# Kernel tuning notes

Hardware: AMD Instinct MI355X
Metric: run time of the kernel (lower is better)

## Reference

```python
import jax, jax.numpy as jnp
import numpy as np

N_NODES = 100000
N_EDGES = 1600000
HIDDEN = 128
HALF = HIDDEN // 2
LN_EPS = 1e-5


def setup_inputs() -> dict:
    key = jax.random.key(0)
    ks = jax.random.split(key, 8)
    pos = jax.random.normal(ks[0], (N_NODES, 3), dtype=jnp.float32) * 10.0
    edge_index = jax.random.randint(ks[1], (2, N_EDGES), 0, N_NODES, dtype=jnp.int64)
    batch = jnp.zeros((N_NODES,), dtype=jnp.int64)
    # spatial_encoder params: Linear(3, HALF) -> LayerNorm(HALF) -> GELU -> Linear(HALF, HALF)
    W1 = jax.random.normal(ks[2], (3, HALF), dtype=jnp.float32) * 0.3
    b1 = jax.random.normal(ks[3], (HALF,), dtype=jnp.float32) * 0.05
    ln_g = jnp.ones((HALF,), dtype=jnp.float32)
    ln_b = jnp.zeros((HALF,), dtype=jnp.float32)
    W2 = jax.random.normal(ks[4], (HALF, HALF), dtype=jnp.float32) * 0.1
    b2 = jax.random.normal(ks[5], (HALF,), dtype=jnp.float32) * 0.05
    return {"pos": pos, "edge_index": edge_index, "batch": batch,
            "W1": W1, "b1": b1, "ln_g": ln_g, "ln_b": ln_b, "W2": W2, "b2": b2}


def _layernorm(x, g, b):
    mu = jnp.mean(x, axis=-1, keepdims=True)
    var = jnp.mean((x - mu) ** 2, axis=-1, keepdims=True)
    return (x - mu) * jax.lax.rsqrt(var + LN_EPS) * g + b


def reference(pos, edge_index, batch, W1, b1, ln_g, ln_b, W2, b2):
    num_nodes = pos.shape[0]
    src, dst = edge_index[0], edge_index[1]
    rel = pos[dst] - pos[src]                              # [E, 3]
    dist = jnp.linalg.norm(rel, axis=1, keepdims=True)     # [E, 1]
    rel_n = rel / (dist + 1e-6)
    h = rel_n @ W1 + b1                                    # [E, HALF]
    h = _layernorm(h, ln_g, ln_b)
    h = jax.nn.gelu(h, approximate=False)                  # torch exact GELU
    code = h @ W2 + b2                                     # dropout is identity in eval
    agg = jax.ops.segment_sum(code, dst, num_segments=num_nodes)          # [N, HALF]
    deg = jax.ops.segment_sum(jnp.ones_like(dst, dtype=code.dtype), dst,
                              num_segments=num_nodes)
    deg = jnp.clip(deg, 1.0)
    agg = agg / deg[:, None]
    # original buffer is [N, HIDDEN]; only the first HALF channels receive updates
    out = jnp.concatenate([agg, jnp.zeros_like(agg)], axis=1)             # [N, HIDDEN]
    return out
```

## Files before the change

kernel.cpp:

```cpp
#include <hip/hip_runtime.h>
#include <math.h>

#define HALF 64
#define LN_EPS 1e-5f
#define SA_CAP 640

#define GC0 -2.3022082f
#define GC1 -0.1029438f

__device__ __forceinline__ float gelu_fast(float x) {
    const float x2 = x * x;
    const float z  = x * fmaf(GC1, x2, GC0);
    const float e  = __builtin_amdgcn_exp2f(z);
    const float sg = __builtin_amdgcn_rcpf(1.0f + e);
    return x * sg;
}

__global__ void __launch_bounds__(256) hist_kernel(
    const int* __restrict__ dst, int* __restrict__ cursor,
    int* __restrict__ rank, int E)
{
    const int e4 = (blockIdx.x * 256 + threadIdx.x) * 4;
    if (e4 + 3 < E) {
        const int4 d = *(const int4*)(dst + e4);
        int4 r;
        r.x = atomicAdd(&cursor[d.x], 1);
        r.y = atomicAdd(&cursor[d.y], 1);
        r.z = atomicAdd(&cursor[d.z], 1);
        r.w = atomicAdd(&cursor[d.w], 1);
        *(int4*)(rank + e4) = r;
    } else {
        for (int e = e4; e < E; ++e) rank[e] = atomicAdd(&cursor[dst[e]], 1);
    }
}

__global__ void __launch_bounds__(1024) scan_kernel(
    const int* __restrict__ cursor, int* __restrict__ offsets,
    int* __restrict__ stat,
    const float* __restrict__ W1, const float* __restrict__ b1,
    float* __restrict__ fp, int N)
{
    const int t = threadIdx.x;
    const int b = blockIdx.x;
    if (b == 0 && t < 64) {
        const float w0 = W1[t], w1 = W1[HALF + t], w2 = W1[2 * HALF + t], bb = b1[t];
        float v[14] = { w0, w1, w2, bb,
                        w0 * w0, w0 * w1, w0 * w2, w1 * w1, w1 * w2, w2 * w2,
                        w0 * bb, w1 * bb, w2 * bb, bb * bb };
#pragma unroll
        for (int j = 0; j < 14; ++j) {
            float s = v[j];
#pragma unroll
            for (int off = 32; off; off >>= 1) s += __shfl_down(s, off, 64);
            if (t == 0) fp[j] = s * (1.0f / 64.0f);
        }
    }

    __shared__ int wtot[16];
    __shared__ int wexc[16];
    __shared__ int stot;
    __shared__ int sPref;
    const int w = t >> 6, lane = t & 63;

    const int i0 = b * 4096 + t * 4;
    int c[4];
    if (i0 + 3 < N) {
        *(int4*)c = *(const int4*)(cursor + i0);
    } else {
#pragma unroll
        for (int j = 0; j < 4; ++j) c[j] = (i0 + j < N) ? cursor[i0 + j] : 0;
    }
    const int s = c[0] + c[1] + c[2] + c[3];
    int incl = s;
#pragma unroll
    for (int off = 1; off < 64; off <<= 1) {
        const int v = __shfl_up(incl, off, 64);
        if (lane >= off) incl += v;
    }
    if (lane == 63) wtot[w] = incl;
    __syncthreads();
    if (t < 16) {
        const int v = wtot[t];
        int inc2 = v;
#pragma unroll
        for (int off = 1; off < 16; off <<= 1) {
            const int u = __shfl_up(inc2, off, 64);
            if (t >= off) inc2 += u;
        }
        wexc[t] = inc2 - v;
        if (t == 15) stot = inc2;
    }
    __syncthreads();

    if (t == 0) {
        const int S = stot;
        if (b == 0) {
            sPref = 0;
            __hip_atomic_store(&stat[0], (S << 2) | 2, __ATOMIC_RELEASE,
                               __HIP_MEMORY_SCOPE_AGENT);
        } else {
            __hip_atomic_store(&stat[b], (S << 2) | 1, __ATOMIC_RELEASE,
                               __HIP_MEMORY_SCOPE_AGENT);
            int running = 0;
            int j = b - 1;
            while (true) {
                const int v = __hip_atomic_load(&stat[j], __ATOMIC_ACQUIRE,
                                                __HIP_MEMORY_SCOPE_AGENT);
                const int st = v & 3;
                if (st == 0) continue;
                running += v >> 2;
                if (st == 2) break;
                --j;
            }
            sPref = running;
            __hip_atomic_store(&stat[b], ((running + S) << 2) | 2,
                               __ATOMIC_RELEASE, __HIP_MEMORY_SCOPE_AGENT);
        }
    }
    __syncthreads();

    int run = sPref + wexc[w] + (incl - s);
#pragma unroll
    for (int j = 0; j < 4; ++j) {
        const int i = i0 + j;
        if (i < N) offsets[i] = run;
        run += c[j];
    }
    if (t == 0 && b == (int)gridDim.x - 1) offsets[N] = sPref + stot;
}

__global__ void __launch_bounds__(256) fillidx_kernel(
    const int* __restrict__ ei, const int* __restrict__ rank,
    const int* __restrict__ offsets, int* __restrict__ srcidx, int E)
{
    const int e4 = (blockIdx.x * 256 + threadIdx.x) * 4;
    if (e4 >= E) return;
    if (e4 + 3 < E) {
        const int4 s = *(const int4*)(ei + e4);
        const int4 d = *(const int4*)(ei + E + e4);
        const int4 r = *(const int4*)(rank + e4);
        srcidx[offsets[d.x] + r.x] = s.x;
        srcidx[offsets[d.y] + r.y] = s.y;
        srcidx[offsets[d.z] + r.z] = s.z;
        srcidx[offsets[d.w] + r.w] = s.w;
    } else {
        for (int e = e4; e < E; ++e)
            srcidx[offsets[ei[E + e]] + rank[e]] = ei[e];
    }
}

__global__ void __launch_bounds__(256, 4) nodeout_kernel(
    const int* __restrict__ srcidx,
    const int* __restrict__ offsets,
    const float* __restrict__ pos,
    const float* __restrict__ W1, const float* __restrict__ b1,
    const float* __restrict__ ln_g, const float* __restrict__ ln_b,
    const float* __restrict__ W2, const float* __restrict__ b2,
    const float* __restrict__ fp,
    float* __restrict__ out, int N)
{
    __shared__ float4 sA[SA_CAP + 8];
    __shared__ float  sh[16 * 64];
    __shared__ int    sOff[17];
    __shared__ float4 sPd[16];

    const int tid = threadIdx.x;
    const int lane = tid & 63, w = tid >> 6;
    const int base = blockIdx.x * 16;

    if (tid < 17) sOff[tid] = offsets[(base + tid < N) ? base + tid : N];
    if (tid < 16) {
        const int n = base + tid;
        if (n < N)
            sPd[tid] = make_float4(pos[3 * n], pos[3 * n + 1], pos[3 * n + 2], 0.0f);
    }

    const float gl = ln_g[lane];
    const float C0 = gl * (W1[lane]            - fp[0]);
    const float C1 = gl * (W1[HALF + lane]     - fp[1]);
    const float C2 = gl * (W1[2 * HALF + lane] - fp[2]);
    const float C3 = gl * (b1[lane]            - fp[3]);
    const float Bl = ln_b[lane];
    const float b2l = b2[lane];

    const float ux = fp[0], uy = fp[1], uz = fp[2], cc = fp[3];
    const float Gxx = fp[4], Gxy = fp[5], Gxz = fp[6];
    const float Gyy = fp[7], Gyz = fp[8], Gzz = fp[9];
    const float px = fp[10], py = fp[11], pz = fp[12], q13 = fp[13];

    const int nend = (base + 16 < N) ? base + 16 : N;
    const int begB = offsets[base];
    const int cntB = offsets[nend] - begB;

    const int n0 = base + w * 4;
    const int o0 = offsets[(n0     < N) ? n0     : N];
    const int o1 = offsets[(n0 + 1 < N) ? n0 + 1 : N];
    const int o2 = offsets[(n0 + 2 < N) ? n0 + 2 : N];
    const int o3 = offsets[(n0 + 3 < N) ? n0 + 3 : N];
    const int o4 = offsets[(n0 + 4 < N) ? n0 + 4 : N];
    const int c0 = o1 - o0, c1 = o2 - o1, c2 = o3 - o2, c3 = o4 - o3;
    const int e1 = c0, e2 = c0 + c1, e3 = c0 + c1 + c2;
    const int wcnt = c0 + c1 + c2 + c3;
    const float i0 = (c0 > 0) ? 1.0f / (float)c0 : 0.0f;
    const float i1 = (c1 > 0) ? 1.0f / (float)c1 : 0.0f;
    const float i2 = (c2 > 0) ? 1.0f / (float)c2 : 0.0f;
    const float i3 = (c3 > 0) ? 1.0f / (float)c3 : 0.0f;
    const int off = o0 - begB;

    __syncthreads();

#define PREPASS(T0, TCNT)                                                   \
    for (int i = tid; i < (TCNT); i += 256) {                               \
        const int slot = begB + (T0) + i;                                   \
        const int s = srcidx[slot];                                         \
        int qd = 0;                                                         \
        _Pragma("unroll")                                                   \
        for (int k = 1; k < 16; ++k) qd += (slot >= sOff[k]) ? 1 : 0;       \
        const float4 pd = sPd[qd];                                          \
        const float rx0 = pd.x - pos[3 * s];                                \
        const float ry0 = pd.y - pos[3 * s + 1];                            \
        const float rz0 = pd.z - pos[3 * s + 2];                            \
        const float dist = sqrtf(rx0 * rx0 + ry0 * ry0 + rz0 * rz0);        \
        const float invd = 1.0f / (dist + 1e-6f);                           \
        const float rx = rx0 * invd, ry = ry0 * invd, rz = rz0 * invd;      \
        const float mu  = fmaf(ux, rx, fmaf(uy, ry, fmaf(uz, rz, cc)));     \
        const float ev2 = Gxx * rx * rx + Gyy * ry * ry + Gzz * rz * rz     \
                        + 2.0f * (Gxy * rx * ry + Gxz * rx * rz             \
                                  + Gyz * ry * rz + px * rx + py * ry       \
                                  + pz * rz) + q13;                         \
        const float rstd = rsqrtf(ev2 - mu * mu + LN_EPS);                  \
        sA[i] = make_float4(rx * rstd, ry * rstd, rz * rstd, rstd);         \
    }

    if (cntB <= SA_CAP) {
        PREPASS(0, cntB)
        __syncthreads();

        int q = 0, nextEnd = e1;
        float accA = 0.0f, accB = 0.0f;
#define FLUSH_ROW()                                                         \
        {                                                                   \
            const float inv = (q == 0) ? i0 : (q == 1) ? i1 : (q == 2) ? i2 : i3; \
            sh[(w * 4 + q) * 64 + lane] = (accA + accB) * inv;              \
            accA = 0.0f; accB = 0.0f; ++q;                                  \
            nextEnd = (q == 1) ? e2 : (q == 2) ? e3 : (q == 3) ? wcnt : 0x7fffffff; \
        }
        for (int i = 0; i < wcnt; i += 8) {
            float4 aa[8];
#pragma unroll
            for (int j = 0; j < 8; ++j) aa[j] = sA[off + i + j];
#pragma unroll
            for (int j = 0; j < 8; ++j) {
                const int idx = i + j;
                while (q < 4 && idx == nextEnd) FLUSH_ROW();
                const float x = fmaf(C0, aa[j].x, fmaf(C1, aa[j].y,
                                  fmaf(C2, aa[j].z, fmaf(C3, aa[j].w, Bl))));
                const float g = gelu_fast(x);
                const float gm = (idx < wcnt) ? g : 0.0f;
                if (j & 1) accB += gm; else accA += gm;
            }
        }
        while (q < 4) FLUSH_ROW();
#undef FLUSH_ROW
    } else {
        float fa0 = 0.0f, fa1 = 0.0f, fa2 = 0.0f, fa3 = 0.0f;
        for (int t0 = 0; t0 < cntB; t0 += SA_CAP) {
            const int tcnt = (cntB - t0 < SA_CAP) ? cntB - t0 : SA_CAP;
            PREPASS(t0, tcnt)
            __syncthreads();
#define ACCUM(FA, LO, HI)                                                   \
            {                                                               \
                int lo = off + (LO); if (lo < t0) lo = t0;                  \
                int hi = off + (HI); if (hi > t0 + tcnt) hi = t0 + tcnt;    \
                for (int i = lo; i < hi; ++i) {                             \
                    const float4 a = sA[i - t0];                            \
                    const float x = fmaf(C0, a.x, fmaf(C1, a.y,             \
                                      fmaf(C2, a.z, fmaf(C3, a.w, Bl))));   \
                    FA += gelu_fast(x);                                     \
                }                                                           \
            }
            ACCUM(fa0, 0,  e1)
            ACCUM(fa1, e1, e2)
            ACCUM(fa2, e2, e3)
            ACCUM(fa3, e3, wcnt)
#undef ACCUM
            __syncthreads();
        }
        sh[(w * 4 + 0) * 64 + lane] = fa0 * i0;
        sh[(w * 4 + 1) * 64 + lane] = fa1 * i1;
        sh[(w * 4 + 2) * 64 + lane] = fa2 * i2;
        sh[(w * 4 + 3) * 64 + lane] = fa3 * i3;
    }
#undef PREPASS

    __builtin_amdgcn_sched_barrier(0);

    float wcol[64];
#pragma unroll
    for (int k = 0; k < 64; ++k) wcol[k] = W2[k * HALF + lane];

#pragma unroll
    for (int qn = 0; qn < 4; ++qn) {
        const int n = n0 + qn;
        if (n < N) {
            const float* shrow = sh + (w * 4 + qn) * 64;
            float oA = 0.0f, oB = 0.0f, oC = 0.0f, oD = 0.0f;
#pragma unroll
            for (int k4 = 0; k4 < 16; ++k4) {
                const float4 hv = *(const float4*)(shrow + k4 * 4);
                oA = fmaf(hv.x, wcol[4 * k4 + 0], oA);
                oB = fmaf(hv.y, wcol[4 * k4 + 1], oB);
                oC = fmaf(hv.z, wcol[4 * k4 + 2], oC);
                oD = fmaf(hv.w, wcol[4 * k4 + 3], oD);
            }
            const int cq = (qn == 0) ? c0 : (qn == 1) ? c1 : (qn == 2) ? c2 : c3;
            const float res = (cq > 0) ? ((oA + oB) + (oC + oD)) + b2l : 0.0f;
            float* orow = out + (size_t)n * (2 * HALF);
            orow[lane] = res;
            orow[HALF + lane] = 0.0f;
        }
    }
}

extern "C" void kernel_launch(void* const* d_in, const int* in_sizes, int n_in,
                              void* d_out, int out_size, void* d_ws, size_t ws_size,
                              hipStream_t stream) {
    const float* pos = (const float*)d_in[0];
    const int*   ei  = (const int*)d_in[1];
    const float* W1  = (const float*)d_in[3];
    const float* b1  = (const float*)d_in[4];
    const float* g   = (const float*)d_in[5];
    const float* b   = (const float*)d_in[6];
    const float* W2  = (const float*)d_in[7];
    const float* b2  = (const float*)d_in[8];
    float* out = (float*)d_out;

    const int N = in_sizes[0] / 3;
    const int E = in_sizes[1] / 2;

    int* srcidx    = (int*)d_ws;
    int* cursor    = srcidx + E + 16;
    int* stat      = cursor + N;
    int* offsets   = stat + 32;
    float* fparams = (float*)(offsets + N + 1);
    int* rank      = (int*)(fparams + 16);

    const int nb = (N + 4095) / 4096;

    hipMemsetAsync(cursor, 0, (size_t)(N + 32) * sizeof(int), stream);
    hist_kernel<<<(E / 4 + 255) / 256, 256, 0, stream>>>(ei + E, cursor, rank, E);
    scan_kernel<<<nb, 1024, 0, stream>>>(cursor, offsets, stat, W1, b1,
                                         fparams, N);
    fillidx_kernel<<<(E / 4 + 255) / 256, 256, 0, stream>>>(ei, rank, offsets,
                                                            srcidx, E);
    nodeout_kernel<<<(N + 15) / 16, 256, 0, stream>>>(srcidx, offsets, pos,
                                                      W1, b1, g, b, W2, b2,
                                                      fparams, out, N);
}
```

Measured before the change: 258.0 us.

## Use packed FP32 math and SoA edge buffers in node output kernel

```diff
diff --git a/kernel.cpp b/kernel.cpp
--- a/kernel.cpp
+++ b/kernel.cpp
@@ -7,6 +7,19 @@
 
 #define GC0 -2.3022082f
 #define GC1 -0.1029438f
+
+typedef float f32x2 __attribute__((ext_vector_type(2)));
+
+__device__ __forceinline__ f32x2 pk_fma(f32x2 a, f32x2 b, f32x2 c) {
+    f32x2 d;
+    asm("v_pk_fma_f32 %0, %1, %2, %3" : "=v"(d) : "v"(a), "v"(b), "v"(c));
+    return d;
+}
+__device__ __forceinline__ f32x2 pk_mul(f32x2 a, f32x2 b) {
+    f32x2 d;
+    asm("v_pk_mul_f32 %0, %1, %2" : "=v"(d) : "v"(a), "v"(b));
+    return d;
+}
 
 __device__ __forceinline__ float gelu_fast(float x) {
     const float x2 = x * x;
@@ -159,8 +172,11 @@
     const float* __restrict__ fp,
     float* __restrict__ out, int N)
 {
-    __shared__ float4 sA[SA_CAP + 8];
-    __shared__ float  sh[16 * 64];
+    __shared__ float sRx[SA_CAP + 8];
+    __shared__ float sRy[SA_CAP + 8];
+    __shared__ float sRz[SA_CAP + 8];
+    __shared__ float sRw[SA_CAP + 8];
+    __shared__ float sh[16 * 64];
     __shared__ int    sOff[17];
     __shared__ float4 sPd[16];
 
@@ -182,6 +198,10 @@
     const float C3 = gl * (b1[lane]            - fp[3]);
     const float Bl = ln_b[lane];
     const float b2l = b2[lane];
+    const f32x2 C0p = { C0, C0 }, C1p = { C1, C1 };
+    const f32x2 C2p = { C2, C2 }, C3p = { C3, C3 };
+    const f32x2 Blp = { Bl, Bl };
+    const f32x2 GC0p = { GC0, GC0 }, GC1p = { GC1, GC1 };
 
     const float ux = fp[0], uy = fp[1], uz = fp[2], cc = fp[3];
     const float Gxx = fp[4], Gxy = fp[5], Gxz = fp[6];
@@ -199,13 +219,6 @@
     const int o3 = offsets[(n0 + 3 < N) ? n0 + 3 : N];
     const int o4 = offsets[(n0 + 4 < N) ? n0 + 4 : N];
     const int c0 = o1 - o0, c1 = o2 - o1, c2 = o3 - o2, c3 = o4 - o3;
-    const int e1 = c0, e2 = c0 + c1, e3 = c0 + c1 + c2;
-    const int wcnt = c0 + c1 + c2 + c3;
-    const float i0 = (c0 > 0) ? 1.0f / (float)c0 : 0.0f;
-    const float i1 = (c1 > 0) ? 1.0f / (float)c1 : 0.0f;
-    const float i2 = (c2 > 0) ? 1.0f / (float)c2 : 0.0f;
-    const float i3 = (c3 > 0) ? 1.0f / (float)c3 : 0.0f;
-    const int off = o0 - begB;
 
     __syncthreads();
 
@@ -229,41 +242,67 @@
                                   + Gyz * ry * rz + px * rx + py * ry       \
                                   + pz * rz) + q13;                         \
         const float rstd = rsqrtf(ev2 - mu * mu + LN_EPS);                  \
-        sA[i] = make_float4(rx * rstd, ry * rstd, rz * rstd, rstd);         \
-    }
+        sRx[i] = rx * rstd;                                                 \
+        sRy[i] = ry * rstd;                                                 \
+        sRz[i] = rz * rstd;                                                 \
+        sRw[i] = rstd;                                                      \
+    }
+
+#define PAIR_LD(V, ARR, IDX)                                                \
+        f32x2 V; V.x = ARR[(IDX)]; V.y = ARR[(IDX) + 1];
+#define PAIR_GELU(RXP, RYP, RZP, RWP, GA, GB)                               \
+        {                                                                   \
+            const f32x2 X = pk_fma(C0p, RXP, pk_fma(C1p, RYP,               \
+                              pk_fma(C2p, RZP, pk_fma(C3p, RWP, Blp))));    \
+            const f32x2 x2 = pk_mul(X, X);                                  \
+            const f32x2 zt = pk_fma(GC1p, x2, GC0p);                        \
+            const f32x2 z  = pk_mul(X, zt);                                 \
+            const float e0 = __builtin_amdgcn_exp2f(z.x);                   \
+            const float e1 = __builtin_amdgcn_exp2f(z.y);                   \
+            const float r0 = __builtin_amdgcn_rcpf(1.0f + e0);              \
+            const float r1 = __builtin_amdgcn_rcpf(1.0f + e1);              \
+            GA += X.x * r0;                                                 \
+            GB += X.y * r1;                                                 \
+        }
 
     if (cntB <= SA_CAP) {
         PREPASS(0, cntB)
         __syncthreads();
 
-        int q = 0, nextEnd = e1;
-        float accA = 0.0f, accB = 0.0f;
-#define FLUSH_ROW()                                                         \
+#define NODE_ACC(OQ, CQ, ROW)                                               \
         {                                                                   \
-            const float inv = (q == 0) ? i0 : (q == 1) ? i1 : (q == 2) ? i2 : i3; \
-            sh[(w * 4 + q) * 64 + lane] = (accA + accB) * inv;              \
-            accA = 0.0f; accB = 0.0f; ++q;                                  \
-            nextEnd = (q == 1) ? e2 : (q == 2) ? e3 : (q == 3) ? wcnt : 0x7fffffff; \
-        }
-        for (int i = 0; i < wcnt; i += 8) {
-            float4 aa[8];
-#pragma unroll
-            for (int j = 0; j < 8; ++j) aa[j] = sA[off + i + j];
-#pragma unroll
-            for (int j = 0; j < 8; ++j) {
-                const int idx = i + j;
-                while (q < 4 && idx == nextEnd) FLUSH_ROW();
-                const float x = fmaf(C0, aa[j].x, fmaf(C1, aa[j].y,
-                                  fmaf(C2, aa[j].z, fmaf(C3, aa[j].w, Bl))));
-                const float g = gelu_fast(x);
-                const float gm = (idx < wcnt) ? g : 0.0f;
-                if (j & 1) accB += gm; else accA += gm;
-            }
-        }
-        while (q < 4) FLUSH_ROW();
-#undef FLUSH_ROW
+            const int cnt = (CQ);                                           \
+            const int bo = (OQ) - begB;                                     \
+            float accA = 0.0f, accB = 0.0f;                                 \
+            int i = 0;                                                      \
+            for (; i + 4 <= cnt; i += 4) {                                  \
+                PAIR_LD(rx0, sRx, bo + i) PAIR_LD(rx1, sRx, bo + i + 2)     \
+                PAIR_LD(ry0, sRy, bo + i) PAIR_LD(ry1, sRy, bo + i + 2)     \
+                PAIR_LD(rz0, sRz, bo + i) PAIR_LD(rz1, sRz, bo + i + 2)     \
+                PAIR_LD(rw0, sRw, bo + i) PAIR_LD(rw1, sRw, bo + i + 2)     \
+                PAIR_GELU(rx0, ry0, rz0, rw0, accA, accB)                   \
+                PAIR_GELU(rx1, ry1, rz1, rw1, accA, accB)                   \
+            }                                                               \
+            for (; i < cnt; ++i) {                                          \
+                const float x = fmaf(C0, sRx[bo + i], fmaf(C1, sRy[bo + i], \
+                                  fmaf(C2, sRz[bo + i],                     \
+                                       fmaf(C3, sRw[bo + i], Bl))));        \
+                accA += gelu_fast(x);                                       \
+            }                                                               \
+            sh[(ROW) * 64 + lane] = (cnt > 0)                               \
+                ? (accA + accB) * (1.0f / (float)cnt) : 0.0f;               \
+        }
+
+        NODE_ACC(o0, c0, w * 4 + 0)
+        NODE_ACC(o1, c1, w * 4 + 1)
+        NODE_ACC(o2, c2, w * 4 + 2)
+        NODE_ACC(o3, c3, w * 4 + 3)
+#undef NODE_ACC
     } else {
         float fa0 = 0.0f, fa1 = 0.0f, fa2 = 0.0f, fa3 = 0.0f;
+        const int off = o0 - begB;
+        const int e1b = c0, e2b = c0 + c1, e3b = c0 + c1 + c2;
+        const int wcnt = c0 + c1 + c2 + c3;
         for (int t0 = 0; t0 < cntB; t0 += SA_CAP) {
             const int tcnt = (cntB - t0 < SA_CAP) ? cntB - t0 : SA_CAP;
             PREPASS(t0, tcnt)
@@ -273,53 +312,58 @@
                 int lo = off + (LO); if (lo < t0) lo = t0;                  \
                 int hi = off + (HI); if (hi > t0 + tcnt) hi = t0 + tcnt;    \
                 for (int i = lo; i < hi; ++i) {                             \
-                    const float4 a = sA[i - t0];                            \
-                    const float x = fmaf(C0, a.x, fmaf(C1, a.y,             \
-                                      fmaf(C2, a.z, fmaf(C3, a.w, Bl))));   \
+                    const int ii = i - t0;                                  \
+                    const float x = fmaf(C0, sRx[ii], fmaf(C1, sRy[ii],     \
+                                      fmaf(C2, sRz[ii],                     \
+                                           fmaf(C3, sRw[ii], Bl))));        \
                     FA += gelu_fast(x);                                     \
                 }                                                           \
             }
-            ACCUM(fa0, 0,  e1)
-            ACCUM(fa1, e1, e2)
-            ACCUM(fa2, e2, e3)
-            ACCUM(fa3, e3, wcnt)
+            ACCUM(fa0, 0,   e1b)
+            ACCUM(fa1, e1b, e2b)
+            ACCUM(fa2, e2b, e3b)
+            ACCUM(fa3, e3b, wcnt)
 #undef ACCUM
             __syncthreads();
         }
-        sh[(w * 4 + 0) * 64 + lane] = fa0 * i0;
-        sh[(w * 4 + 1) * 64 + lane] = fa1 * i1;
-        sh[(w * 4 + 2) * 64 + lane] = fa2 * i2;
-        sh[(w * 4 + 3) * 64 + lane] = fa3 * i3;
+        sh[(w * 4 + 0) * 64 + lane] = (c0 > 0) ? fa0 / (float)c0 : 0.0f;
+        sh[(w * 4 + 1) * 64 + lane] = (c1 > 0) ? fa1 / (float)c1 : 0.0f;
+        sh[(w * 4 + 2) * 64 + lane] = (c2 > 0) ? fa2 / (float)c2 : 0.0f;
+        sh[(w * 4 + 3) * 64 + lane] = (c3 > 0) ? fa3 / (float)c3 : 0.0f;
     }
 #undef PREPASS
+#undef PAIR_GELU
+#undef PAIR_LD
 
     __builtin_amdgcn_sched_barrier(0);
 
-    float wcol[64];
-#pragma unroll
-    for (int k = 0; k < 64; ++k) wcol[k] = W2[k * HALF + lane];
-
-#pragma unroll
-    for (int qn = 0; qn < 4; ++qn) {
-        const int n = n0 + qn;
-        if (n < N) {
-            const float* shrow = sh + (w * 4 + qn) * 64;
-            float oA = 0.0f, oB = 0.0f, oC = 0.0f, oD = 0.0f;
-#pragma unroll
-            for (int k4 = 0; k4 < 16; ++k4) {
-                const float4 hv = *(const float4*)(shrow + k4 * 4);
-                oA = fmaf(hv.x, wcol[4 * k4 + 0], oA);
-                oB = fmaf(hv.y, wcol[4 * k4 + 1], oB);
-                oC = fmaf(hv.z, wcol[4 * k4 + 2], oC);
-                oD = fmaf(hv.w, wcol[4 * k4 + 3], oD);
-            }
-            const int cq = (qn == 0) ? c0 : (qn == 1) ? c1 : (qn == 2) ? c2 : c3;
-            const float res = (cq > 0) ? ((oA + oB) + (oC + oD)) + b2l : 0.0f;
-            float* orow = out + (size_t)n * (2 * HALF);
-            orow[lane] = res;
-            orow[HALF + lane] = 0.0f;
-        }
-    }
+    f32x2 wpk[32];
+#pragma unroll
+    for (int k = 0; k < 32; ++k) {
+        wpk[k].x = W2[(2 * k)     * HALF + lane];
+        wpk[k].y = W2[(2 * k + 1) * HALF + lane];
+    }
+
+#define PHASE2(Q, CQ)                                                       \
+    if (n0 + (Q) < N) {                                                     \
+        const float* row = sh + (w * 4 + (Q)) * 64;                         \
+        f32x2 acc = { 0.0f, 0.0f };                                         \
+        _Pragma("unroll")                                                   \
+        for (int k = 0; k < 32; ++k) {                                      \
+            f32x2 h; h.x = row[2 * k]; h.y = row[2 * k + 1];                \
+            acc = pk_fma(h, wpk[k], acc);                                   \
+        }                                                                   \
+        const float res = ((CQ) > 0) ? (acc.x + acc.y) + b2l : 0.0f;        \
+        float* orow = out + (size_t)(n0 + (Q)) * (2 * HALF);                \
+        orow[lane] = res;                                                   \
+        orow[HALF + lane] = 0.0f;                                           \
+    }
+
+    PHASE2(0, c0)
+    PHASE2(1, c1)
+    PHASE2(2, c2)
+    PHASE2(3, c3)
+#undef PHASE2
 }
 
 extern "C" void kernel_launch(void* const* d_in, const int* in_sizes, int n_in,
@@ -346,13 +390,13 @@
     int* rank      = (int*)(fparams + 16);
 
     const int nb = (N + 4095) / 4096;
+    const int eb4 = (E / 4 + 255) / 256;
 
     hipMemsetAsync(cursor, 0, (size_t)(N + 32) * sizeof(int), stream);
-    hist_kernel<<<(E / 4 + 255) / 256, 256, 0, stream>>>(ei + E, cursor, rank, E);
+    hist_kernel<<<eb4, 256, 0, stream>>>(ei + E, cursor, rank, E);
     scan_kernel<<<nb, 1024, 0, stream>>>(cursor, offsets, stat, W1, b1,
                                          fparams, N);
-    fillidx_kernel<<<(E / 4 + 255) / 256, 256, 0, stream>>>(ei, rank, offsets,
-                                                            srcidx, E);
+    fillidx_kernel<<<eb4, 256, 0, stream>>>(ei, rank, offsets, srcidx, E);
     nodeout_kernel<<<(N + 15) / 16, 256, 0, stream>>>(srcidx, offsets, pos,
                                                       W1, b1, g, b, W2, b2,
                                                       fparams, out, N);
```

Result: faster. 252.5 us (-2.1%).
